# Optimization experiments

Hardware: AMD Instinct MI355X
Metric: run time of the kernel (lower is better)

## Reference

```python
import jax, jax.numpy as jnp
import numpy as np
from jax import lax

WIN = 5
WIN_SIZE = float(WIN * WIN * WIN)


def _box_sum(x):
    # 5x5x5 all-ones box-filter sum, stride 1, padding 2 (SAME), single channel.
    k = jnp.ones((1, 1, WIN, WIN, WIN), dtype=x.dtype)
    return lax.conv_general_dilated(
        x, k,
        window_strides=(1, 1, 1),
        padding=[(2, 2), (2, 2), (2, 2)],
        dimension_numbers=('NCDHW', 'OIDHW', 'NCDHW'))


def setup_inputs() -> dict:
    key = jax.random.key(0)
    k1, k2 = jax.random.split(key)
    shape = (2, 1, 160, 160, 160)
    real = jax.random.normal(k1, shape, dtype=jnp.float32)
    fake = jax.random.normal(k2, shape, dtype=jnp.float32)
    return {"real": real, "fake": fake}


def reference(real, fake):
    I2 = real * real
    J2 = fake * fake
    IJ = real * fake
    I_sum = _box_sum(real)
    J_sum = _box_sum(fake)
    I2_sum = _box_sum(I2)
    J2_sum = _box_sum(J2)
    IJ_sum = _box_sum(IJ)
    u_I = I_sum / WIN_SIZE
    u_J = J_sum / WIN_SIZE
    cross = IJ_sum - u_J * I_sum - u_I * J_sum + u_I * u_J * WIN_SIZE
    I_var = I2_sum - 2.0 * u_I * I_sum + u_I * u_I * WIN_SIZE
    J_var = J2_sum - 2.0 * u_J * J_sum + u_J * u_J * WIN_SIZE
    cc = cross * cross / (I_var * J_var + 1e-05)
    return jnp.mean(cc)
```

## Files before the change

kernel.cpp:

```cpp
#include <hip/hip_runtime.h>


#define DIM 160
#define SLAB (DIM * DIM)
#define VOL (DIM * DIM * DIM)
#define TD 8
#define ROWS 36
#define RST 44
#define VOFF (ROWS * RST)
#define NBLK 1000
#define NPART (NBLK * 4)

typedef float f4 __attribute__((ext_vector_type(4), aligned(16)));
typedef float f2 __attribute__((ext_vector_type(2), aligned(8)));

__device__ __forceinline__ f2 hw2(const f2 r0, const f2 r1, const f2 r2) {
    const float c = (r0.y + r1.x) + r1.y;
    return (f2){(r0.x + c) + r2.x, (c + r2.x) + r2.y};
}

__global__ __launch_bounds__(256, 2) void ncc_main(const float* __restrict__ real,
                                                   const float* __restrict__ fake,
                                                   float* __restrict__ partials) {
    __shared__ __align__(16) float raw[2][2][ROWS][RST];

    const int tid = threadIdx.x;

    const int bid = blockIdx.x;
    const int vid = (bid & 7) * 125 + (bid >> 3);
    const int dz  = vid % 20;
    const int t1  = vid / 20;
    const int bx  = t1 % 5;
    const int by  = (t1 / 5) % 5;
    const int nb  = t1 / 25;
    const int w0 = 32 * bx, h0 = 32 * by, d0 = TD * dz;

    const float* baseI = real + (size_t)nb * VOL;
    const float* baseJ = fake + (size_t)nb * VOL;

    const int sc = tid & 15;
    const int sr = tid >> 4;
    const int co = (2 * sr) * RST + 2 * sc + 2;

    int gof[3], lof[3];
    bool ok[3];
    const float* src[3];
#pragma unroll
    for (int k = 0; k < 3; ++k) {
        const int t   = tid + 256 * k;
        const int tv  = t / 360;
        const int rem = t - 360 * tv;
        const int row = rem / 10;
        const int q   = rem - 10 * row;
        const int hg  = h0 - 2 + row;
        const int wq  = w0 - 4 + 4 * q;
        ok[k]  = (t < 720) && ((unsigned)hg < DIM) && (wq >= 0) && (wq + 3 < DIM);
        gof[k] = hg * DIM + wq;
        lof[k] = (tv * ROWS + row) * RST + 4 * q;
        src[k] = tv ? baseJ : baseI;
    }

    {
        float* L = &raw[0][0][0][0];
        for (int i = tid; i < 2 * 2 * ROWS * RST / 4; i += 256)
            *(f4*)(L + 4 * i) = (f4){0.f, 0.f, 0.f, 0.f};
    }
    __syncthreads();

    if (d0 > 0) {
        const size_t so = (size_t)(d0 - 2) * SLAB;
        float* L = &raw[0][0][0][0];
#pragma unroll
        for (int k = 0; k < 3; ++k)
            if (ok[k]) *(f4*)(L + lof[k]) = *(const f4*)(src[k] + so + gof[k]);
    }
    __syncthreads();

    const f2 z2 = (f2){0.f, 0.f};
    const f4 zf = (f4){0.f, 0.f, 0.f, 0.f};
    f2 zr0[5][5], zr1[5][5];
#pragma unroll
    for (int p = 0; p < 5; ++p)
#pragma unroll
        for (int q = 0; q < 5; ++q) { zr0[p][q] = z2; zr1[p][q] = z2; }

    f2 acc = z2;
    const float inv = 1.0f / 125.0f;
    int cur = 0;

#pragma unroll 1
    for (int a = 0; a < 3; ++a) {
        const bool am0 = (a > 0);
#pragma unroll
        for (int b = 0; b < 5; ++b) {
            const bool compAct  = (a < 2) || (b < 2);
            const bool stageAct = (a < 2) || (b == 0);
            if (!compAct) continue;

            f4 v0 = zf, v1 = zf, v2 = zf;
            if (stageAct) {
                const int dd1 = d0 - 1 + 5 * a + b;
                if ((unsigned)dd1 < DIM) {
                    const size_t so = (size_t)dd1 * SLAB;
                    if (ok[0]) v0 = *(const f4*)(src[0] + so + gof[0]);
                    if (ok[1]) v1 = *(const f4*)(src[1] + so + gof[1]);
                    if (ok[2]) v2 = *(const f4*)(src[2] + so + gof[2]);
                }
            }

            const float* LB = &raw[cur][0][0][0];
            f2 c00 = z2, c01 = z2, c02 = z2, c03 = z2, c04 = z2;
            f2 c10 = z2, c11 = z2, c12 = z2, c13 = z2, c14 = z2;
#pragma unroll
            for (int t = 0; t < 6; ++t) {
                const float* rp = LB + co + t * RST;
                const f2 a0 = *(const f2*)(rp);
                const f2 a1 = *(const f2*)(rp + 2);
                const f2 a2 = *(const f2*)(rp + 4);
                const f2 b0 = *(const f2*)(rp + VOFF);
                const f2 b1 = *(const f2*)(rp + VOFF + 2);
                const f2 b2 = *(const f2*)(rp + VOFF + 4);
                const f2 w0v = hw2(a0, a1, a2);
                const f2 w1v = hw2(b0, b1, b2);
                const f2 w2v = hw2(a0 * a0, a1 * a1, a2 * a2);
                const f2 w3v = hw2(b0 * b0, b1 * b1, b2 * b2);
                const f2 w4v = hw2(a0 * b0, a1 * b1, a2 * b2);
                if (t < 5) { c00 += w0v; c01 += w1v; c02 += w2v; c03 += w3v; c04 += w4v; }
                if (t > 0) { c10 += w0v; c11 += w1v; c12 += w2v; c13 += w3v; c14 += w4v; }
            }

#pragma unroll
            for (int p = 0; p < 5; ++p) {
                const int kk  = (b - p + 5) % 5;
                const int bmk = b - kk;
                const bool doadd = (am0 || p <= b) &&
                                   (a == 0 || (a == 1 ? (bmk <= 2) : (bmk <= -3)));
                if (doadd) {
                    zr0[p][0] += c00; zr0[p][1] += c01; zr0[p][2] += c02;
                    zr0[p][3] += c03; zr0[p][4] += c04;
                    zr1[p][0] += c10; zr1[p][1] += c11; zr1[p][2] += c12;
                    zr1[p][3] += c13; zr1[p][4] += c14;
                }
            }

            const bool docomp = (a == 0) ? (b == 4) : ((a == 1) ? true : (b < 2));
            if (docomp) {
                const int pe = (b + 1) % 5;
                {
                    const f2 SI = zr0[pe][0], SJ = zr0[pe][1];
                    const f2 S2I = zr0[pe][2], S2J = zr0[pe][3], SIJ = zr0[pe][4];
                    const f2 t0    = SI * inv;
                    const f2 cross = SIJ - t0 * SJ;
                    const f2 iv    = S2I - t0 * SI;
                    const f2 jv    = S2J - (SJ * inv) * SJ;
                    acc += cross * cross / (iv * jv + 1e-5f);
                    zr0[pe][0] = z2; zr0[pe][1] = z2; zr0[pe][2] = z2;
                    zr0[pe][3] = z2; zr0[pe][4] = z2;
                }
                {
                    const f2 SI = zr1[pe][0], SJ = zr1[pe][1];
                    const f2 S2I = zr1[pe][2], S2J = zr1[pe][3], SIJ = zr1[pe][4];
                    const f2 t0    = SI * inv;
                    const f2 cross = SIJ - t0 * SJ;
                    const f2 iv    = S2I - t0 * SI;
                    const f2 jv    = S2J - (SJ * inv) * SJ;
                    acc += cross * cross / (iv * jv + 1e-5f);
                    zr1[pe][0] = z2; zr1[pe][1] = z2; zr1[pe][2] = z2;
                    zr1[pe][3] = z2; zr1[pe][4] = z2;
                }
            }

            if (stageAct) {
                float* LW = &raw[cur ^ 1][0][0][0];
                if (ok[0]) *(f4*)(LW + lof[0]) = v0;
                if (ok[1]) *(f4*)(LW + lof[1]) = v1;
                if (ok[2]) *(f4*)(LW + lof[2]) = v2;
            }
            __syncthreads();
            cur ^= 1;
        }
    }

    float a2 = acc.x + acc.y;
#pragma unroll
    for (int off = 32; off; off >>= 1)
        a2 += __shfl_down(a2, off, 64);
    if ((tid & 63) == 0)
        partials[bid * 4 + (tid >> 6)] = a2;
}

__global__ void ncc_reduce(const float* __restrict__ partials, float* __restrict__ out) {
    __shared__ double ws[4];
    double s = 0.0;
    for (int i = threadIdx.x; i < NPART; i += 256) s += (double)partials[i];
#pragma unroll
    for (int off = 32; off; off >>= 1)
        s += __shfl_down(s, off, 64);
    if ((threadIdx.x & 63) == 0) ws[threadIdx.x >> 6] = s;
    __syncthreads();
    if (threadIdx.x == 0) {
        const double t = ws[0] + ws[1] + ws[2] + ws[3];
        out[0] = (float)(t / (2.0 * (double)VOL));
    }
}

extern "C" void kernel_launch(void* const* d_in, const int* in_sizes, int n_in,
                              void* d_out, int out_size, void* d_ws, size_t ws_size,
                              hipStream_t stream) {
    const float* real = (const float*)d_in[0];
    const float* fake = (const float*)d_in[1];
    float* out      = (float*)d_out;
    float* partials = (float*)d_ws;

    ncc_main<<<dim3(NBLK), dim3(256), 0, stream>>>(real, fake, partials);
    ncc_reduce<<<1, 256, 0, stream>>>(partials, out);
}
```

Before: 55.91 us.

## Use single-wave blocks with smaller row tiles to replace block barriers

Each block shrinks from 256 threads covering 32x32x8 outputs to one 64-lane wavefront covering 32x8x8 outputs, so there are four times as many blocks. Because a block is now a single wave, the per-slab __syncthreads calls become wave barriers, which removes the cross-wave stalls on every depth step. The cost is a larger halo relative to the tile (12 staged rows for 8 output rows instead of 36 for 32), which means more redundant global and LDS loads per output.

```diff
diff --git a/kernel.cpp b/kernel.cpp
--- a/kernel.cpp
+++ b/kernel.cpp
@@ -5,11 +5,11 @@
 #define SLAB (DIM * DIM)
 #define VOL (DIM * DIM * DIM)
 #define TD 8
-#define ROWS 36
+#define ROWS 12
 #define RST 44
 #define VOFF (ROWS * RST)
-#define NBLK 1000
-#define NPART (NBLK * 4)
+#define NBLK 4000
+#define NPART NBLK
 
 typedef float f4 __attribute__((ext_vector_type(4), aligned(16)));
 typedef float f2 __attribute__((ext_vector_type(2), aligned(8)));
@@ -19,62 +19,62 @@
     return (f2){(r0.x + c) + r2.x, (c + r2.x) + r2.y};
 }
 
-__global__ __launch_bounds__(256, 2) void ncc_main(const float* __restrict__ real,
-                                                   const float* __restrict__ fake,
-                                                   float* __restrict__ partials) {
+__global__ __launch_bounds__(64, 4) void ncc_main(const float* __restrict__ real,
+                                                  const float* __restrict__ fake,
+                                                  float* __restrict__ partials) {
     __shared__ __align__(16) float raw[2][2][ROWS][RST];
 
-    const int tid = threadIdx.x;
+    const int lane = threadIdx.x;
 
     const int bid = blockIdx.x;
-    const int vid = (bid & 7) * 125 + (bid >> 3);
+    const int vid = (bid & 7) * 500 + (bid >> 3);
     const int dz  = vid % 20;
     const int t1  = vid / 20;
     const int bx  = t1 % 5;
-    const int by  = (t1 / 5) % 5;
-    const int nb  = t1 / 25;
-    const int w0 = 32 * bx, h0 = 32 * by, d0 = TD * dz;
+    const int by  = (t1 / 5) % 20;
+    const int nb  = t1 / 100;
+    const int w0 = 32 * bx, h0 = 8 * by, d0 = TD * dz;
 
     const float* baseI = real + (size_t)nb * VOL;
     const float* baseJ = fake + (size_t)nb * VOL;
 
-    const int sc = tid & 15;
-    const int sr = tid >> 4;
+    const int sc = lane & 15;
+    const int sr = lane >> 4;
     const int co = (2 * sr) * RST + 2 * sc + 2;
 
-    int gof[3], lof[3];
-    bool ok[3];
-    const float* src[3];
-#pragma unroll
-    for (int k = 0; k < 3; ++k) {
-        const int t   = tid + 256 * k;
-        const int tv  = t / 360;
-        const int rem = t - 360 * tv;
+    int gof[4], lof[4];
+    bool ok[4];
+    const float* src[4];
+#pragma unroll
+    for (int k = 0; k < 4; ++k) {
+        const int t   = lane + 64 * k;
+        const int tv  = t / 120;
+        const int rem = t - 120 * tv;
         const int row = rem / 10;
         const int q   = rem - 10 * row;
         const int hg  = h0 - 2 + row;
         const int wq  = w0 - 4 + 4 * q;
-        ok[k]  = (t < 720) && ((unsigned)hg < DIM) && (wq >= 0) && (wq + 3 < DIM);
+        ok[k]  = (t < 240) && ((unsigned)hg < DIM) && (wq >= 0) && (wq + 3 < DIM);
         gof[k] = hg * DIM + wq;
-        lof[k] = (tv * ROWS + row) * RST + 4 * q;
-        src[k] = tv ? baseJ : baseI;
+        lof[k] = ((tv < 2 ? tv : 0) * ROWS + row) * RST + 4 * q;
+        src[k] = (tv == 1) ? baseJ : baseI;
     }
 
     {
         float* L = &raw[0][0][0][0];
-        for (int i = tid; i < 2 * 2 * ROWS * RST / 4; i += 256)
+        for (int i = lane; i < 2 * 2 * ROWS * RST / 4; i += 64)
             *(f4*)(L + 4 * i) = (f4){0.f, 0.f, 0.f, 0.f};
     }
-    __syncthreads();
+    __builtin_amdgcn_wave_barrier();
 
     if (d0 > 0) {
         const size_t so = (size_t)(d0 - 2) * SLAB;
         float* L = &raw[0][0][0][0];
 #pragma unroll
-        for (int k = 0; k < 3; ++k)
+        for (int k = 0; k < 4; ++k)
             if (ok[k]) *(f4*)(L + lof[k]) = *(const f4*)(src[k] + so + gof[k]);
     }
-    __syncthreads();
+    __builtin_amdgcn_wave_barrier();
 
     const f2 z2 = (f2){0.f, 0.f};
     const f4 zf = (f4){0.f, 0.f, 0.f, 0.f};
@@ -97,7 +97,7 @@
             const bool stageAct = (a < 2) || (b == 0);
             if (!compAct) continue;
 
-            f4 v0 = zf, v1 = zf, v2 = zf;
+            f4 v0 = zf, v1 = zf, v2 = zf, v3 = zf;
             if (stageAct) {
                 const int dd1 = d0 - 1 + 5 * a + b;
                 if ((unsigned)dd1 < DIM) {
@@ -105,6 +105,7 @@
                     if (ok[0]) v0 = *(const f4*)(src[0] + so + gof[0]);
                     if (ok[1]) v1 = *(const f4*)(src[1] + so + gof[1]);
                     if (ok[2]) v2 = *(const f4*)(src[2] + so + gof[2]);
+                    if (ok[3]) v3 = *(const f4*)(src[3] + so + gof[3]);
                 }
             }
 
@@ -170,13 +171,16 @@
                 }
             }
 
+            __builtin_amdgcn_wave_barrier();
+
             if (stageAct) {
                 float* LW = &raw[cur ^ 1][0][0][0];
                 if (ok[0]) *(f4*)(LW + lof[0]) = v0;
                 if (ok[1]) *(f4*)(LW + lof[1]) = v1;
                 if (ok[2]) *(f4*)(LW + lof[2]) = v2;
-            }
-            __syncthreads();
+                if (ok[3]) *(f4*)(LW + lof[3]) = v3;
+            }
+            __builtin_amdgcn_wave_barrier();
             cur ^= 1;
         }
     }
@@ -185,8 +189,8 @@
 #pragma unroll
     for (int off = 32; off; off >>= 1)
         a2 += __shfl_down(a2, off, 64);
-    if ((tid & 63) == 0)
-        partials[bid * 4 + (tid >> 6)] = a2;
+    if (lane == 0)
+        partials[bid] = a2;
 }
 
 __global__ void ncc_reduce(const float* __restrict__ partials, float* __restrict__ out) {
@@ -212,6 +216,6 @@
     float* out      = (float*)d_out;
     float* partials = (float*)d_ws;
 
-    ncc_main<<<dim3(NBLK), dim3(256), 0, stream>>>(real, fake, partials);
+    ncc_main<<<dim3(NBLK), dim3(64), 0, stream>>>(real, fake, partials);
     ncc_reduce<<<1, 256, 0, stream>>>(partials, out);
 }
```

Result: slower. 175.3 us (+213.5%).
